# Kernel optimization log

Measured on AMD Instinct MI355X. Metric: run time of the kernel, lower is better.

## Reference

```python
import jax, jax.numpy as jnp
import numpy as np

B, T, D, NH, F = 8, 1024, 1152, 16, 4304
HD = D // NH


def _ln(x, w, b, eps=1e-5):
    m = jnp.mean(x, axis=-1, keepdims=True)
    v = jnp.mean((x - m) ** 2, axis=-1, keepdims=True)
    return (x - m) * jax.lax.rsqrt(v + eps) * w + b


def setup_inputs() -> dict:
    key = jax.random.key(0)
    ks = jax.random.split(key, 8)
    s = 0.02
    return {
        "x": jax.random.normal(ks[0], (B, T, D), jnp.float32),
        "ln1_w": jnp.ones((D,), jnp.float32),
        "ln1_b": jnp.zeros((D,), jnp.float32),
        "wq": jax.random.normal(ks[1], (D, D), jnp.float32) * s,
        "bq": jnp.zeros((D,), jnp.float32),
        "wk": jax.random.normal(ks[2], (D, D), jnp.float32) * s,
        "bk": jnp.zeros((D,), jnp.float32),
        "wv": jax.random.normal(ks[3], (D, D), jnp.float32) * s,
        "bv": jnp.zeros((D,), jnp.float32),
        "wo": jax.random.normal(ks[4], (D, D), jnp.float32) * s,
        "bo": jnp.zeros((D,), jnp.float32),
        "ln2_w": jnp.ones((D,), jnp.float32),
        "ln2_b": jnp.zeros((D,), jnp.float32),
        "w1": jax.random.normal(ks[5], (F, D), jnp.float32) * s,
        "b1": jnp.zeros((F,), jnp.float32),
        "w2": jax.random.normal(ks[6], (D, F), jnp.float32) * s,
        "b2": jnp.zeros((D,), jnp.float32),
    }


def reference(x, ln1_w, ln1_b, wq, bq, wk, bk, wv, bv, wo, bo,
              ln2_w, ln2_b, w1, b1, w2, b2):
    b, t, d = x.shape
    h = _ln(x, ln1_w, ln1_b)
    q = h @ wq.T + bq
    k = h @ wk.T + bk
    v = h @ wv.T + bv
    # Faithful to torch: .view(B, H, T, hd) with NO transpose (non-standard split)
    q = q.reshape(b, NH, t, HD)
    k = k.reshape(b, NH, t, HD)
    v = v.reshape(b, NH, t, HD)
    scale = HD ** -0.5
    att = jnp.einsum('bhtd,bhsd->bhts', q, k) * scale  # [B,H,T,T]
    scores = jax.nn.softmax(att, axis=-1)  # dropout skipped (eval mode)
    o = jnp.einsum('bhts,bhsd->bhtd', scores, v)
    o = o.transpose(0, 2, 1, 3).reshape(b, t, d)  # transpose(1,2) + flatten(2)
    o = o @ wo.T + bo
    x1 = o + x
    h2 = _ln(x1, ln2_w, ln2_b)
    f = jax.nn.gelu(h2 @ w1.T + b1, approximate=True)
    return f @ w2.T + b2 + x1
```

## Files before the change

### kernel.cpp

```cpp
#include <hip/hip_runtime.h>
#include <cstddef>
#include <cstdint>


constexpr int kB = 8, kT = 1024, kD = 1152, kNH = 16, kF = 4304, kHD = 72;
constexpr int kNT = kB * kT;
constexpr int kFP = 4352;
constexpr int kEP = 96;
constexpr int kEV = 80;
constexpr int kFC = 2176;

typedef short bf16x8 __attribute__((ext_vector_type(8)));
typedef float f32x4 __attribute__((ext_vector_type(4)));

__device__ __forceinline__ ushort f2bf(float f) {
  union { float f; uint u; } a; a.f = f;
  const uint r = a.u + 0x7FFFu + ((a.u >> 16) & 1u);
  return (ushort)(r >> 16);
}
__device__ __forceinline__ float gelu_tanh(float x) {
  const float u = 0.7978845608028654f * (x + 0.044715f * x * x * x);
  return 0.5f * x * (1.0f + tanhf(u));
}
#define GLL16(g, s) __builtin_amdgcn_global_load_lds( \
    (const __attribute__((address_space(1))) void*)(g), \
    (__attribute__((address_space(3))) void*)(s), 16, 0, 0)

__global__ __launch_bounds__(256) void ln_kernel(const float* __restrict__ in,
                                                 const float* __restrict__ w,
                                                 const float* __restrict__ b,
                                                 ushort* __restrict__ out) {
  const int row = blockIdx.x;
  const float4* r4 = reinterpret_cast<const float4*>(in + (size_t)row * kD);
  const float4* w4 = reinterpret_cast<const float4*>(w);
  const float4* b4 = reinterpret_cast<const float4*>(b);
  const int t = threadIdx.x;
  float4 v0 = r4[t];
  float4 v1 = make_float4(0.f, 0.f, 0.f, 0.f);
  const bool second = (t < kD / 4 - 256);
  if (second) v1 = r4[t + 256];
  float s  = v0.x + v0.y + v0.z + v0.w + v1.x + v1.y + v1.z + v1.w;
  float ss = v0.x * v0.x + v0.y * v0.y + v0.z * v0.z + v0.w * v0.w +
             v1.x * v1.x + v1.y * v1.y + v1.z * v1.z + v1.w * v1.w;
  #pragma unroll
  for (int m = 1; m <= 32; m <<= 1) { s += __shfl_xor(s, m); ss += __shfl_xor(ss, m); }
  __shared__ float red[8];
  const int wave = t >> 6;
  if ((t & 63) == 0) { red[wave] = s; red[4 + wave] = ss; }
  __syncthreads();
  s  = red[0] + red[1] + red[2] + red[3];
  ss = red[4] + red[5] + red[6] + red[7];
  const float mean = s * (1.0f / kD);
  const float var  = ss * (1.0f / kD) - mean * mean;
  const float rs   = rsqrtf(var + 1e-5f);
  ushort4* o4 = reinterpret_cast<ushort4*>(out + (size_t)row * kD);
  {
    float4 W = w4[t], Bv = b4[t];
    ushort4 r;
    r.x = f2bf((v0.x - mean) * rs * W.x + Bv.x);
    r.y = f2bf((v0.y - mean) * rs * W.y + Bv.y);
    r.z = f2bf((v0.z - mean) * rs * W.z + Bv.z);
    r.w = f2bf((v0.w - mean) * rs * W.w + Bv.w);
    o4[t] = r;
  }
  if (second) {
    float4 W = w4[t + 256], Bv = b4[t + 256];
    ushort4 r;
    r.x = f2bf((v1.x - mean) * rs * W.x + Bv.x);
    r.y = f2bf((v1.y - mean) * rs * W.y + Bv.y);
    r.z = f2bf((v1.z - mean) * rs * W.z + Bv.z);
    r.w = f2bf((v1.w - mean) * rs * W.w + Bv.w);
    o4[t + 256] = r;
  }
}

__global__ __launch_bounds__(256) void cvt4_kernel(const float* __restrict__ src,
                                                   ushort* __restrict__ dst, int n4) {
  const int i = blockIdx.x * 256 + threadIdx.x;
  if (i < n4) {
    const float4 v = reinterpret_cast<const float4*>(src)[i];
    ushort4 r = { f2bf(v.x), f2bf(v.y), f2bf(v.z), f2bf(v.w) };
    reinterpret_cast<ushort4*>(dst)[i] = r;
  }
}
__global__ __launch_bounds__(256) void cvtw2_kernel(const float* __restrict__ src,
                                                    ushort* __restrict__ dst) {
  const int i = blockIdx.x * 256 + threadIdx.x;
  if (i >= kD * (kFP / 4)) return;
  const int r = i / (kFP / 4), c4 = i % (kFP / 4);
  const int c = c4 * 4;
  ushort4 o;
  if (c < kF) {
    const float4 v = *reinterpret_cast<const float4*>(src + (size_t)r * kF + c);
    o = { f2bf(v.x), f2bf(v.y), f2bf(v.z), f2bf(v.w) };
  } else o = { 0, 0, 0, 0 };
  reinterpret_cast<ushort4*>(dst + (size_t)r * kFP)[c4] = o;
}
__global__ __launch_bounds__(256) void b1pad_kernel(const float* __restrict__ src,
                                                    float* __restrict__ dst) {
  const int i = blockIdx.x * 256 + threadIdx.x;
  if (i < kFP) dst[i] = (i < kF) ? src[i] : 0.f;
}
__global__ __launch_bounds__(256) void zfill_kernel(ushort* __restrict__ kp,
                                                    ushort* __restrict__ vt) {
  const int i = blockIdx.x * 256 + threadIdx.x;
  const int nk = 131072 * 24;
  if (i < nk) {
    const int row = i / 24, c = 72 + i % 24;
    kp[(size_t)row * kEP + c] = 0;
  } else {
    const int j = i - nk;
    if (j < 131072 * 8) {
      const int bh = j >> 13, rem = j & 8191;
      const int e = 72 + (rem >> 10), s = rem & 1023;
      vt[((size_t)bh * kEV + e) * 1024 + s] = 0;
    }
  }
}

template <int MODE, int GELU_, int BIAS_, int RES_, int SCALE_>
__global__ __launch_bounds__(256) void gemm_mfma(
    const ushort* __restrict__ A, const ushort* __restrict__ W,
    const float* __restrict__ bias, const float* __restrict__ res,
    void* __restrict__ Cout, int M, int K, int ldw) {
  __shared__ __align__(16) ushort As[128 * 32];
  __shared__ __align__(16) ushort Bs[128 * 32];
  const int tid = threadIdx.x;
  const int l = tid & 63, w = tid >> 6;
  const int lr = l & 15, lg = l >> 4;
  const int wm = w >> 1, wn = w & 1;
  const int bn = blockIdx.x, bm = blockIdx.y;
  f32x4 acc[4][4] = {};
  const int srow = 32 * w + (l >> 2);
  const int scol = (l & 3) * 8;
  const ushort* Ag = A + (size_t)(bn * 128 + srow) * K + scol;
  const ushort* Wg = W + (size_t)(bm * 128 + srow) * ldw + scol;
  for (int k0 = 0; k0 < K; k0 += 32) {
    __syncthreads();
    #pragma unroll
    for (int i = 0; i < 2; i++) {
      GLL16(Ag + (size_t)(16 * i) * K + k0, &As[(32 * w + 16 * i) * 32]);
      GLL16(Wg + (size_t)(16 * i) * ldw + k0, &Bs[(32 * w + 16 * i) * 32]);
    }
    __syncthreads();
    bf16x8 af[4], bf[4];
    #pragma unroll
    for (int mf = 0; mf < 4; mf++)
      af[mf] = *(const bf16x8*)&As[(wm * 64 + mf * 16 + lr) * 32 + lg * 8];
    #pragma unroll
    for (int nf = 0; nf < 4; nf++)
      bf[nf] = *(const bf16x8*)&Bs[(wn * 64 + nf * 16 + lr) * 32 + lg * 8];
    #pragma unroll
    for (int mf = 0; mf < 4; mf++)
      #pragma unroll
      for (int nf = 0; nf < 4; nf++)
        acc[mf][nf] = __builtin_amdgcn_mfma_f32_16x16x32_bf16(af[mf], bf[nf], acc[mf][nf], 0, 0, 0);
  }
  #pragma unroll
  for (int mf = 0; mf < 4; mf++) {
    #pragma unroll
    for (int nf = 0; nf < 4; nf++) {
      const int c = bm * 128 + wn * 64 + nf * 16 + lr;
      const float bv = BIAS_ ? bias[c] : 0.f;
      #pragma unroll
      for (int j = 0; j < 4; j++) {
        const int r = bn * 128 + wm * 64 + mf * 16 + lg * 4 + j;
        float v = acc[mf][nf][j] + bv;
        if (SCALE_) v *= 0.11785113019775793f;
        if (GELU_) v = gelu_tanh(v);
        if (RES_) v += res[(size_t)r * M + c];
        if (MODE == 0) {
          ((float*)Cout)[(size_t)r * M + c] = v;
        } else if (MODE == 1) {
          ((ushort*)Cout)[(size_t)r * M + c] = f2bf(v);
        } else {
          const int b = r >> 10, t = r & 1023;
          const int h = t >> 6, u = t & 63;
          const int jj = c / 72, e = c - jj * 72;
          const int s = u * 16 + jj;
          const int bh = b * 16 + h;
          size_t dst;
          if (MODE == 2) dst = ((size_t)bh * 1024 + s) * kEP + e;
          else           dst = ((size_t)bh * kEV + e) * 1024 + s;
          ((ushort*)Cout)[dst] = f2bf(v);
        }
      }
    }
  }
}

__global__ __launch_bounds__(256, 2) void attn_kernel(
    const ushort* __restrict__ qp, const ushort* __restrict__ kp,
    const ushort* __restrict__ vt, ushort* __restrict__ ob) {
  __shared__ __align__(16) ushort Kt[64 * 96];
  __shared__ __align__(16) ushort Vt[80 * 64];
  __shared__ __align__(16) ushort Ps[4][64 * 72];
  const int tid = threadIdx.x, l = tid & 63, w = tid >> 6;
  const int lr = l & 15, lg = l >> 4;
  const int qb = blockIdx.x, hh = blockIdx.y, bb = blockIdx.z;
  const int bh = bb * 16 + hh;
  const int s0 = qb * 256 + w * 64;
  bf16x8 qf[4][3];
  const ushort* qbase = qp + (size_t)bh * 1024 * kEP;
  #pragma unroll
  for (int mf = 0; mf < 4; mf++)
    #pragma unroll
    for (int ks = 0; ks < 3; ks++)
      qf[mf][ks] = *(const bf16x8*)(qbase + (size_t)(s0 + mf * 16 + lr) * kEP + ks * 32 + lg * 8);
  float mstate[16], lstate[16];
  #pragma unroll
  for (int i = 0; i < 16; i++) { mstate[i] = -1e30f; lstate[i] = 0.f; }
  f32x4 oacc[4][5] = {};
  const ushort* ktile0 = kp + (size_t)bh * 1024 * kEP;
  const ushort* vbase  = vt + (size_t)bh * kEV * 1024;
  ushort* myPs = &Ps[w][0];

  for (int kt = 0; kt < 16; kt++) {
    __syncthreads();
    {
      const ushort* kg = ktile0 + (size_t)kt * 64 * kEP;
      #pragma unroll
      for (int i = 0; i < 3; i++) {
        const int is = w * 3 + i;
        GLL16(kg + is * 512 + l * 8, &Kt[is * 512]);
      }
    }
    {
      #pragma unroll
      for (int i = 0; i < 3; i++) {
        const int is = w + i * 4;
        if (is < 10) {
          const int e = is * 8 + (l >> 3);
          const int cg = (l & 7) ^ (e & 7);
          GLL16(vbase + (size_t)e * 1024 + kt * 64 + cg * 8, &Vt[is * 512]);
        }
      }
    }
    __syncthreads();
    f32x4 sacc[4][4];
    #pragma unroll
    for (int mf = 0; mf < 4; mf++)
      #pragma unroll
      for (int nf = 0; nf < 4; nf++)
        sacc[mf][nf] = (f32x4){0.f, 0.f, 0.f, 0.f};
    #pragma unroll
    for (int ks = 0; ks < 3; ks++) {
      bf16x8 kf[4];
      #pragma unroll
      for (int nf = 0; nf < 4; nf++)
        kf[nf] = *(const bf16x8*)&Kt[(nf * 16 + lr) * 96 + ks * 32 + lg * 8];
      #pragma unroll
      for (int mf = 0; mf < 4; mf++)
        #pragma unroll
        for (int nf = 0; nf < 4; nf++)
          sacc[mf][nf] = __builtin_amdgcn_mfma_f32_16x16x32_bf16(qf[mf][ks], kf[nf], sacc[mf][nf], 0, 0, 0);
    }
    #pragma unroll
    for (int mf = 0; mf < 4; mf++) {
      float alpha[4];
      #pragma unroll
      for (int j = 0; j < 4; j++) {
        float v = fmaxf(fmaxf(sacc[mf][0][j], sacc[mf][1][j]),
                        fmaxf(sacc[mf][2][j], sacc[mf][3][j]));
        v = fmaxf(v, __shfl_xor(v, 1));
        v = fmaxf(v, __shfl_xor(v, 2));
        v = fmaxf(v, __shfl_xor(v, 4));
        v = fmaxf(v, __shfl_xor(v, 8));
        const int si = mf * 4 + j;
        const float mo = mstate[si];
        const float mn = fmaxf(mo, v);
        float sum = 0.f;
        #pragma unroll
        for (int nf = 0; nf < 4; nf++) {
          const float p = __expf(sacc[mf][nf][j] - mn);
          sacc[mf][nf][j] = p;
          sum += p;
        }
        sum += __shfl_xor(sum, 1);
        sum += __shfl_xor(sum, 2);
        sum += __shfl_xor(sum, 4);
        sum += __shfl_xor(sum, 8);
        alpha[j] = __expf(mo - mn);
        lstate[si] = lstate[si] * alpha[j] + sum;
        mstate[si] = mn;
      }
      #pragma unroll
      for (int nf = 0; nf < 5; nf++)
        #pragma unroll
        for (int j = 0; j < 4; j++)
          oacc[mf][nf][j] *= alpha[j];
      #pragma unroll
      for (int nf = 0; nf < 4; nf++)
        #pragma unroll
        for (int j = 0; j < 4; j++)
          myPs[(mf * 16 + lg * 4 + j) * 72 + nf * 16 + lr] = f2bf(sacc[mf][nf][j]);
    }
    #pragma unroll
    for (int mf = 0; mf < 4; mf++) {
      bf16x8 pa0 = *(const bf16x8*)&myPs[(mf * 16 + lr) * 72 + lg * 8];
      bf16x8 pa1 = *(const bf16x8*)&myPs[(mf * 16 + lr) * 72 + 32 + lg * 8];
      #pragma unroll
      for (int nf = 0; nf < 5; nf++) {
        const int e = nf * 16 + lr;
        const int sw = e & 7;
        bf16x8 vb0 = *(const bf16x8*)&Vt[e * 64 + ((0 + lg) ^ sw) * 8];
        bf16x8 vb1 = *(const bf16x8*)&Vt[e * 64 + ((4 + lg) ^ sw) * 8];
        oacc[mf][nf] = __builtin_amdgcn_mfma_f32_16x16x32_bf16(pa0, vb0, oacc[mf][nf], 0, 0, 0);
        oacc[mf][nf] = __builtin_amdgcn_mfma_f32_16x16x32_bf16(pa1, vb1, oacc[mf][nf], 0, 0, 0);
      }
    }
  }
  float linv[16];
  #pragma unroll
  for (int i = 0; i < 16; i++) linv[i] = 1.f / lstate[i];
  #pragma unroll
  for (int mf = 0; mf < 4; mf++)
    #pragma unroll
    for (int nf = 0; nf < 5; nf++) {
      const int e = nf * 16 + lr;
      if (e < 72) {
        #pragma unroll
        for (int j = 0; j < 4; j++) {
          const int s = s0 + mf * 16 + lg * 4 + j;
          ob[((size_t)bb * 1024 + s) * kD + hh * kHD + e] =
              f2bf(oacc[mf][nf][j] * linv[mf * 4 + j]);
        }
      }
    }
}

extern "C" void kernel_launch(void* const* d_in, const int* in_sizes, int n_in,
                              void* d_out, int out_size, void* d_ws, size_t ws_size,
                              hipStream_t stream) {
  const float* x    = (const float*)d_in[0];
  const float* ln1w = (const float*)d_in[1];
  const float* ln1b = (const float*)d_in[2];
  const float* wq   = (const float*)d_in[3];
  const float* bq   = (const float*)d_in[4];
  const float* wk   = (const float*)d_in[5];
  const float* bk   = (const float*)d_in[6];
  const float* wv   = (const float*)d_in[7];
  const float* bv   = (const float*)d_in[8];
  const float* wo   = (const float*)d_in[9];
  const float* bo   = (const float*)d_in[10];
  const float* ln2w = (const float*)d_in[11];
  const float* ln2b = (const float*)d_in[12];
  const float* w1   = (const float*)d_in[13];
  const float* b1   = (const float*)d_in[14];
  const float* w2   = (const float*)d_in[15];
  const float* b2   = (const float*)d_in[16];
  float* out = (float*)d_out;

  ushort* ws = (ushort*)d_ws;
  const size_t nD = (size_t)kNT * kD;
  const size_t nQK = (size_t)kB * kNH * 1024 * kEP;
  const size_t nVT = (size_t)kB * kNH * kEV * 1024;
  ushort* hb  = ws;
  ushort* qp  = hb + nD;
  ushort* kp  = qp + nQK;
  ushort* vt  = kp + nQK;
  ushort* wqb = vt + nVT;
  ushort* wkb = wqb + (size_t)kD * kD;
  ushort* wvb = wkb + (size_t)kD * kD;
  ushort* wob = wvb + (size_t)kD * kD;
  ushort* w1b = wob + (size_t)kD * kD;
  ushort* w2b = w1b + (size_t)kFP * kD;
  float*  x1  = (float*)(w2b + (size_t)kD * kFP);
  float*  b1b = x1 + nD;
  ushort* ob  = hb;
  ushort* h2b = qp;
  ushort* fb  = kp;

  const dim3 blk(256);
  const dim3 gqkv(64, 9);
  const dim3 gm1(64, 17);
  const dim3 ga(4, 16, 8);

  const int nDD4 = kD * kD / 4;
  cvt4_kernel<<<(nDD4 + 255) / 256, blk, 0, stream>>>(wq, wqb, nDD4);
  cvt4_kernel<<<(nDD4 + 255) / 256, blk, 0, stream>>>(wk, wkb, nDD4);
  cvt4_kernel<<<(nDD4 + 255) / 256, blk, 0, stream>>>(wv, wvb, nDD4);
  cvt4_kernel<<<(nDD4 + 255) / 256, blk, 0, stream>>>(wo, wob, nDD4);
  const int nW14 = kF * kD / 4;
  cvt4_kernel<<<(nW14 + 255) / 256, blk, 0, stream>>>(w1, w1b, nW14);
  cvtw2_kernel<<<(kD * (kFP / 4) + 255) / 256, blk, 0, stream>>>(w2, w2b);
  b1pad_kernel<<<(kFP + 255) / 256, blk, 0, stream>>>(b1, b1b);
  zfill_kernel<<<16384, blk, 0, stream>>>(kp, vt);

  ln_kernel<<<kNT, blk, 0, stream>>>(x, ln1w, ln1b, hb);
  gemm_mfma<2, 0, 1, 0, 1><<<gqkv, blk, 0, stream>>>(hb, wqb, bq, nullptr, qp, kD, kD, kD);
  gemm_mfma<2, 0, 1, 0, 0><<<gqkv, blk, 0, stream>>>(hb, wkb, bk, nullptr, kp, kD, kD, kD);
  gemm_mfma<3, 0, 1, 0, 0><<<gqkv, blk, 0, stream>>>(hb, wvb, bv, nullptr, vt, kD, kD, kD);
  attn_kernel<<<ga, blk, 0, stream>>>(qp, kp, vt, ob);
  gemm_mfma<0, 0, 1, 1, 0><<<gqkv, blk, 0, stream>>>(ob, wob, bo, x, x1, kD, kD, kD);
  ln_kernel<<<kNT, blk, 0, stream>>>(x1, ln2w, ln2b, h2b);
  gemm_mfma<1, 1, 1, 0, 0><<<gm1, blk, 0, stream>>>(h2b, w1b, b1b, nullptr, fb, kFC, kD, kD);
  gemm_mfma<0, 0, 1, 1, 0><<<gqkv, blk, 0, stream>>>(fb, w2b, b2, x1, out, kD, kFC, kFP);
  gemm_mfma<1, 1, 1, 0, 0><<<gm1, blk, 0, stream>>>(h2b, w1b + (size_t)kFC * kD, b1b + kFC, nullptr, fb, kFC, kD, kD);
  gemm_mfma<0, 0, 0, 1, 0><<<gqkv, blk, 0, stream>>>(fb, w2b + kFC, nullptr, out, out, kD, kFC, kFP);
}
```

Baseline: 982.3 us.

## Fuse QKV projections into one GEMM and keep attention P in registers

Merges the three Q/K/V projection GEMMs into a single launch with a 27-row-block grid, choosing bias, output buffer and layout per projection in the epilogue. Attention now computes S transposed, so the softmax row reductions need fewer shuffles. The P matrix is repacked into MFMA A-operand layout with cross-lane shuffles instead of an LDS round trip, which removes the Ps shared buffer and its traffic. The change also zero-fills the w1 padding rows, and it adds shuffle and select overhead plus a more complex epilogue.

Measured after the change: 873.6 us. 1.12x faster.

```diff
diff --git a/kernel.cpp b/kernel.cpp
--- a/kernel.cpp
+++ b/kernel.cpp
@@ -97,9 +97,12 @@
   reinterpret_cast<ushort4*>(dst + (size_t)r * kFP)[c4] = o;
 }
 __global__ __launch_bounds__(256) void b1pad_kernel(const float* __restrict__ src,
-                                                    float* __restrict__ dst) {
+                                                    float* __restrict__ dst,
+                                                    ushort* __restrict__ w1b) {
   const int i = blockIdx.x * 256 + threadIdx.x;
   if (i < kFP) dst[i] = (i < kF) ? src[i] : 0.f;
+  const int j = i - kFP;
+  if (j >= 0 && j < (kFP - kF) * kD) w1b[(size_t)kF * kD + j] = 0;
 }
 __global__ __launch_bounds__(256) void zfill_kernel(ushort* __restrict__ kp,
                                                     ushort* __restrict__ vt) {
@@ -118,11 +121,13 @@
   }
 }
 
-template <int MODE, int GELU_, int BIAS_, int RES_, int SCALE_>
+template <int MODE, int GELU_, int BIAS_, int RES_>
 __global__ __launch_bounds__(256) void gemm_mfma(
     const ushort* __restrict__ A, const ushort* __restrict__ W,
-    const float* __restrict__ bias, const float* __restrict__ res,
-    void* __restrict__ Cout, int M, int K, int ldw) {
+    const float* __restrict__ bias, const float* __restrict__ bias2,
+    const float* __restrict__ bias3, const float* __restrict__ res,
+    void* __restrict__ Cout, void* __restrict__ C2, void* __restrict__ C3,
+    int M, int K, int ldw) {
   __shared__ __align__(16) ushort As[128 * 32];
   __shared__ __align__(16) ushort Bs[128 * 32];
   const int tid = threadIdx.x;
@@ -132,7 +137,7 @@
   const int bn = blockIdx.x, bm = blockIdx.y;
   f32x4 acc[4][4] = {};
   const int srow = 32 * w + (l >> 2);
-  const int scol = (l & 3) * 8;
+  const int scol = (l & 3) << 3;
   const ushort* Ag = A + (size_t)(bn * 128 + srow) * K + scol;
   const ushort* Wg = W + (size_t)(bm * 128 + srow) * ldw + scol;
   for (int k0 = 0; k0 < K; k0 += 32) {
@@ -156,6 +161,34 @@
       for (int nf = 0; nf < 4; nf++)
         acc[mf][nf] = __builtin_amdgcn_mfma_f32_16x16x32_bf16(af[mf], bf[nf], acc[mf][nf], 0, 0, 0);
   }
+  if (MODE == 4) {
+    const int proj = bm / 9;
+    const float* bp = proj == 0 ? bias : (proj == 1 ? bias2 : bias3);
+    ushort* dstp = (ushort*)(proj == 0 ? Cout : (proj == 1 ? C2 : C3));
+    #pragma unroll
+    for (int mf = 0; mf < 4; mf++) {
+      #pragma unroll
+      for (int nf = 0; nf < 4; nf++) {
+        const int c = bm * 128 + wn * 64 + nf * 16 + lr;
+        const int cl = c - proj * kD;
+        const int jj = cl / 72, e = cl - jj * 72;
+        const float bv = bp[cl];
+        #pragma unroll
+        for (int j = 0; j < 4; j++) {
+          const int r = bn * 128 + wm * 64 + mf * 16 + lg * 4 + j;
+          float v = acc[mf][nf][j] + bv;
+          if (proj == 0) v *= 0.11785113019775793f;
+          const int b = r >> 10, t = r & 1023;
+          const int h = t >> 6, u = t & 63;
+          const int s = u * 16 + jj, bh = b * 16 + h;
+          const size_t dst = (proj < 2) ? ((size_t)bh * 1024 + s) * kEP + e
+                                        : ((size_t)bh * kEV + e) * 1024 + s;
+          dstp[dst] = f2bf(v);
+        }
+      }
+    }
+    return;
+  }
   #pragma unroll
   for (int mf = 0; mf < 4; mf++) {
     #pragma unroll
@@ -166,24 +199,10 @@
       for (int j = 0; j < 4; j++) {
         const int r = bn * 128 + wm * 64 + mf * 16 + lg * 4 + j;
         float v = acc[mf][nf][j] + bv;
-        if (SCALE_) v *= 0.11785113019775793f;
         if (GELU_) v = gelu_tanh(v);
         if (RES_) v += res[(size_t)r * M + c];
-        if (MODE == 0) {
-          ((float*)Cout)[(size_t)r * M + c] = v;
-        } else if (MODE == 1) {
-          ((ushort*)Cout)[(size_t)r * M + c] = f2bf(v);
-        } else {
-          const int b = r >> 10, t = r & 1023;
-          const int h = t >> 6, u = t & 63;
-          const int jj = c / 72, e = c - jj * 72;
-          const int s = u * 16 + jj;
-          const int bh = b * 16 + h;
-          size_t dst;
-          if (MODE == 2) dst = ((size_t)bh * 1024 + s) * kEP + e;
-          else           dst = ((size_t)bh * kEV + e) * 1024 + s;
-          ((ushort*)Cout)[dst] = f2bf(v);
-        }
+        if (MODE == 0) ((float*)Cout)[(size_t)r * M + c] = v;
+        else           ((ushort*)Cout)[(size_t)r * M + c] = f2bf(v);
       }
     }
   }
@@ -194,7 +213,6 @@
     const ushort* __restrict__ vt, ushort* __restrict__ ob) {
   __shared__ __align__(16) ushort Kt[64 * 96];
   __shared__ __align__(16) ushort Vt[80 * 64];
-  __shared__ __align__(16) ushort Ps[4][64 * 72];
   const int tid = threadIdx.x, l = tid & 63, w = tid >> 6;
   const int lr = l & 15, lg = l >> 4;
   const int qb = blockIdx.x, hh = blockIdx.y, bb = blockIdx.z;
@@ -203,17 +221,20 @@
   bf16x8 qf[4][3];
   const ushort* qbase = qp + (size_t)bh * 1024 * kEP;
   #pragma unroll
-  for (int mf = 0; mf < 4; mf++)
+  for (int qi = 0; qi < 4; qi++)
     #pragma unroll
     for (int ks = 0; ks < 3; ks++)
-      qf[mf][ks] = *(const bf16x8*)(qbase + (size_t)(s0 + mf * 16 + lr) * kEP + ks * 32 + lg * 8);
-  float mstate[16], lstate[16];
+      qf[qi][ks] = *(const bf16x8*)(qbase + (size_t)(s0 + qi * 16 + lr) * kEP + ks * 32 + lg * 8);
+  float mstate[4], lstate[4];
   #pragma unroll
-  for (int i = 0; i < 16; i++) { mstate[i] = -1e30f; lstate[i] = 0.f; }
+  for (int i = 0; i < 4; i++) { mstate[i] = -1e30f; lstate[i] = 0.f; }
   f32x4 oacc[4][5] = {};
   const ushort* ktile0 = kp + (size_t)bh * 1024 * kEP;
   const ushort* vbase  = vt + (size_t)bh * kEV * 1024;
-  ushort* myPs = &Ps[w][0];
+  const int srcA = lr + 32 * (lg & 1);
+  const int srcB = srcA + 16;
+  const int hi = lg >> 1;
+  const int rmap = (lg << 4) + (lg << 2);
 
   for (int kt = 0; kt < 16; kt++) {
     __syncthreads();
@@ -239,94 +260,101 @@
     __syncthreads();
     f32x4 sacc[4][4];
     #pragma unroll
-    for (int mf = 0; mf < 4; mf++)
-      #pragma unroll
-      for (int nf = 0; nf < 4; nf++)
-        sacc[mf][nf] = (f32x4){0.f, 0.f, 0.f, 0.f};
+    for (int si = 0; si < 4; si++)
+      #pragma unroll
+      for (int qi = 0; qi < 4; qi++)
+        sacc[si][qi] = (f32x4){0.f, 0.f, 0.f, 0.f};
     #pragma unroll
     for (int ks = 0; ks < 3; ks++) {
       bf16x8 kf[4];
       #pragma unroll
-      for (int nf = 0; nf < 4; nf++)
-        kf[nf] = *(const bf16x8*)&Kt[(nf * 16 + lr) * 96 + ks * 32 + lg * 8];
-      #pragma unroll
-      for (int mf = 0; mf < 4; mf++)
-        #pragma unroll
-        for (int nf = 0; nf < 4; nf++)
-          sacc[mf][nf] = __builtin_amdgcn_mfma_f32_16x16x32_bf16(qf[mf][ks], kf[nf], sacc[mf][nf], 0, 0, 0);
-    }
-    #pragma unroll
-    for (int mf = 0; mf < 4; mf++) {
-      float alpha[4];
-      #pragma unroll
-      for (int j = 0; j < 4; j++) {
-        float v = fmaxf(fmaxf(sacc[mf][0][j], sacc[mf][1][j]),
-                        fmaxf(sacc[mf][2][j], sacc[mf][3][j]));
-        v = fmaxf(v, __shfl_xor(v, 1));
-        v = fmaxf(v, __shfl_xor(v, 2));
-        v = fmaxf(v, __shfl_xor(v, 4));
-        v = fmaxf(v, __shfl_xor(v, 8));
-        const int si = mf * 4 + j;
-        const float mo = mstate[si];
-        const float mn = fmaxf(mo, v);
-        float sum = 0.f;
-        #pragma unroll
-        for (int nf = 0; nf < 4; nf++) {
-          const float p = __expf(sacc[mf][nf][j] - mn);
-          sacc[mf][nf][j] = p;
+      for (int si = 0; si < 4; si++)
+        kf[si] = *(const bf16x8*)&Kt[(si * 16 + lr) * 96 + ks * 32 + lg * 8];
+      #pragma unroll
+      for (int si = 0; si < 4; si++)
+        #pragma unroll
+        for (int qi = 0; qi < 4; qi++)
+          sacc[si][qi] = __builtin_amdgcn_mfma_f32_16x16x32_bf16(kf[si], qf[qi][ks], sacc[si][qi], 0, 0, 0);
+    }
+    #pragma unroll
+    for (int qi = 0; qi < 4; qi++) {
+      float mx = sacc[0][qi][0];
+      #pragma unroll
+      for (int si = 0; si < 4; si++)
+        #pragma unroll
+        for (int j = 0; j < 4; j++) mx = fmaxf(mx, sacc[si][qi][j]);
+      mx = fmaxf(mx, __shfl_xor(mx, 16));
+      mx = fmaxf(mx, __shfl_xor(mx, 32));
+      const float mo = mstate[qi], mn = fmaxf(mo, mx);
+      float sum = 0.f;
+      #pragma unroll
+      for (int si = 0; si < 4; si++)
+        #pragma unroll
+        for (int j = 0; j < 4; j++) {
+          const float p = __expf(sacc[si][qi][j] - mn);
+          sacc[si][qi][j] = p;
           sum += p;
         }
-        sum += __shfl_xor(sum, 1);
-        sum += __shfl_xor(sum, 2);
-        sum += __shfl_xor(sum, 4);
-        sum += __shfl_xor(sum, 8);
-        alpha[j] = __expf(mo - mn);
-        lstate[si] = lstate[si] * alpha[j] + sum;
-        mstate[si] = mn;
-      }
-      #pragma unroll
-      for (int nf = 0; nf < 5; nf++)
-        #pragma unroll
-        for (int j = 0; j < 4; j++)
-          oacc[mf][nf][j] *= alpha[j];
-      #pragma unroll
-      for (int nf = 0; nf < 4; nf++)
-        #pragma unroll
-        for (int j = 0; j < 4; j++)
-          myPs[(mf * 16 + lg * 4 + j) * 72 + nf * 16 + lr] = f2bf(sacc[mf][nf][j]);
-    }
-    #pragma unroll
-    for (int mf = 0; mf < 4; mf++) {
-      bf16x8 pa0 = *(const bf16x8*)&myPs[(mf * 16 + lr) * 72 + lg * 8];
-      bf16x8 pa1 = *(const bf16x8*)&myPs[(mf * 16 + lr) * 72 + 32 + lg * 8];
-      #pragma unroll
-      for (int nf = 0; nf < 5; nf++) {
-        const int e = nf * 16 + lr;
+      sum += __shfl_xor(sum, 16);
+      sum += __shfl_xor(sum, 32);
+      const float al = __expf(mo - mn);
+      lstate[qi] = lstate[qi] * al + sum;
+      mstate[qi] = mn;
+      #pragma unroll
+      for (int j = 0; j < 4; j++) {
+        const float alj = __shfl(al, rmap + j);
+        #pragma unroll
+        for (int ei = 0; ei < 5; ei++) oacc[qi][ei][j] *= alj;
+      }
+      uint wlo[4], whi[4];
+      #pragma unroll
+      for (int si = 0; si < 4; si++) {
+        wlo[si] = (uint)f2bf(sacc[si][qi][0]) | ((uint)f2bf(sacc[si][qi][1]) << 16);
+        whi[si] = (uint)f2bf(sacc[si][qi][2]) | ((uint)f2bf(sacc[si][qi][3]) << 16);
+      }
+      uint A0[4], A1[4], A2[4], A3[4];
+      #pragma unroll
+      for (int si = 0; si < 4; si++) {
+        A0[si] = (uint)__shfl((int)wlo[si], srcA);
+        A1[si] = (uint)__shfl((int)whi[si], srcA);
+        A2[si] = (uint)__shfl((int)wlo[si], srcB);
+        A3[si] = (uint)__shfl((int)whi[si], srcB);
+      }
+      union U { uint u[4]; bf16x8 v; } p0, p1;
+      p0.u[0] = hi ? A0[1] : A0[0];  p0.u[1] = hi ? A1[1] : A1[0];
+      p0.u[2] = hi ? A2[1] : A2[0];  p0.u[3] = hi ? A3[1] : A3[0];
+      p1.u[0] = hi ? A0[3] : A0[2];  p1.u[1] = hi ? A1[3] : A1[2];
+      p1.u[2] = hi ? A2[3] : A2[2];  p1.u[3] = hi ? A3[3] : A3[2];
+      #pragma unroll
+      for (int ei = 0; ei < 5; ei++) {
+        const int e = ei * 16 + lr;
         const int sw = e & 7;
         bf16x8 vb0 = *(const bf16x8*)&Vt[e * 64 + ((0 + lg) ^ sw) * 8];
         bf16x8 vb1 = *(const bf16x8*)&Vt[e * 64 + ((4 + lg) ^ sw) * 8];
-        oacc[mf][nf] = __builtin_amdgcn_mfma_f32_16x16x32_bf16(pa0, vb0, oacc[mf][nf], 0, 0, 0);
-        oacc[mf][nf] = __builtin_amdgcn_mfma_f32_16x16x32_bf16(pa1, vb1, oacc[mf][nf], 0, 0, 0);
-      }
-    }
-  }
-  float linv[16];
+        oacc[qi][ei] = __builtin_amdgcn_mfma_f32_16x16x32_bf16(p0.v, vb0, oacc[qi][ei], 0, 0, 0);
+        oacc[qi][ei] = __builtin_amdgcn_mfma_f32_16x16x32_bf16(p1.v, vb1, oacc[qi][ei], 0, 0, 0);
+      }
+    }
+  }
   #pragma unroll
-  for (int i = 0; i < 16; i++) linv[i] = 1.f / lstate[i];
-  #pragma unroll
-  for (int mf = 0; mf < 4; mf++)
-    #pragma unroll
-    for (int nf = 0; nf < 5; nf++) {
-      const int e = nf * 16 + lr;
+  for (int qi = 0; qi < 4; qi++) {
+    const float rli = 1.f / lstate[qi];
+    float lij[4];
+    #pragma unroll
+    for (int j = 0; j < 4; j++) lij[j] = __shfl(rli, rmap + j);
+    #pragma unroll
+    for (int ei = 0; ei < 5; ei++) {
+      const int e = ei * 16 + lr;
       if (e < 72) {
         #pragma unroll
         for (int j = 0; j < 4; j++) {
-          const int s = s0 + mf * 16 + lg * 4 + j;
+          const int s = s0 + qi * 16 + lg * 4 + j;
           ob[((size_t)bb * 1024 + s) * kD + hh * kHD + e] =
-              f2bf(oacc[mf][nf][j] * linv[mf * 4 + j]);
+              f2bf(oacc[qi][ei][j] * lij[j]);
         }
       }
     }
+  }
 }
 
 extern "C" void kernel_launch(void* const* d_in, const int* in_sizes, int n_in,
@@ -372,7 +400,8 @@
   ushort* fb  = kp;
 
   const dim3 blk(256);
-  const dim3 gqkv(64, 9);
+  const dim3 gqkv(64, 27);
+  const dim3 go(64, 9);
   const dim3 gm1(64, 17);
   const dim3 ga(4, 16, 8);
 
@@ -384,18 +413,23 @@
   const int nW14 = kF * kD / 4;
   cvt4_kernel<<<(nW14 + 255) / 256, blk, 0, stream>>>(w1, w1b, nW14);
   cvtw2_kernel<<<(kD * (kFP / 4) + 255) / 256, blk, 0, stream>>>(w2, w2b);
-  b1pad_kernel<<<(kFP + 255) / 256, blk, 0, stream>>>(b1, b1b);
+  b1pad_kernel<<<(kFP + (kFP - kF) * kD + 255) / 256, blk, 0, stream>>>(b1, b1b, w1b);
   zfill_kernel<<<16384, blk, 0, stream>>>(kp, vt);
 
   ln_kernel<<<kNT, blk, 0, stream>>>(x, ln1w, ln1b, hb);
-  gemm_mfma<2, 0, 1, 0, 1><<<gqkv, blk, 0, stream>>>(hb, wqb, bq, nullptr, qp, kD, kD, kD);
-  gemm_mfma<2, 0, 1, 0, 0><<<gqkv, blk, 0, stream>>>(hb, wkb, bk, nullptr, kp, kD, kD, kD);
-  gemm_mfma<3, 0, 1, 0, 0><<<gqkv, blk, 0, stream>>>(hb, wvb, bv, nullptr, vt, kD, kD, kD);
+  gemm_mfma<4, 0, 1, 0><<<gqkv, blk, 0, stream>>>(hb, wqb, bq, bk, bv, nullptr,
+                                                  qp, kp, vt, kD, kD, kD);
   attn_kernel<<<ga, blk, 0, stream>>>(qp, kp, vt, ob);
-  gemm_mfma<0, 0, 1, 1, 0><<<gqkv, blk, 0, stream>>>(ob, wob, bo, x, x1, kD, kD, kD);
+  gemm_mfma<0, 0, 1, 1><<<go, blk, 0, stream>>>(ob, wob, bo, nullptr, nullptr, x,
+                                                x1, nullptr, nullptr, kD, kD, kD);
   ln_kernel<<<kNT, blk, 0, stream>>>(x1, ln2w, ln2b, h2b);
-  gemm_mfma<1, 1, 1, 0, 0><<<gm1, blk, 0, stream>>>(h2b, w1b, b1b, nullptr, fb, kFC, kD, kD);
-  gemm_mfma<0, 0, 1, 1, 0><<<gqkv, blk, 0, stream>>>(fb, w2b, b2, x1, out, kD, kFC, kFP);
-  gemm_mfma<1, 1, 1, 0, 0><<<gm1, blk, 0, stream>>>(h2b, w1b + (size_t)kFC * kD, b1b + kFC, nullptr, fb, kFC, kD, kD);
-  gemm_mfma<0, 0, 0, 1, 0><<<gqkv, blk, 0, stream>>>(fb, w2b + kFC, nullptr, out, out, kD, kFC, kFP);
-}
+  gemm_mfma<1, 1, 1, 0><<<gm1, blk, 0, stream>>>(h2b, w1b, b1b, nullptr, nullptr, nullptr,
+                                                 fb, nullptr, nullptr, kFC, kD, kD);
+  gemm_mfma<0, 0, 1, 1><<<go, blk, 0, stream>>>(fb, w2b, b2, nullptr, nullptr, x1,
+                                                out, nullptr, nullptr, kD, kFC, kFP);
+  gemm_mfma<1, 1, 1, 0><<<gm1, blk, 0, stream>>>(h2b, w1b + (size_t)kFC * kD, b1b + kFC,
+                                                 nullptr, nullptr, nullptr,
+                                                 fb, nullptr, nullptr, kFC, kD, kD);
+  gemm_mfma<0, 0, 0, 1><<<go, blk, 0, stream>>>(fb, w2b + kFC, nullptr, nullptr, nullptr,
+                                                out, out, nullptr, nullptr, kD, kFC, kFP);
+}
```
